# Kernel optimization log

Hardware: AMD Instinct MI355X
Metric: run time of the kernel (lower is better)

## Reference

```python
import jax, jax.numpy as jnp
import numpy as np

B = 4096          # batch
F = 1024          # feature_count * embedding_dim
E = 16            # embedding_dim (domain embedding)
D = 8             # num_domains
T = F + E         # cross-net total dim
L = 3             # cross layers
EPS = 1e-5


def setup_inputs() -> dict:
    key = jax.random.key(0)
    ks = jax.random.split(key, 32)
    s = 0.02
    inp = {}
    inp["x"] = jax.random.normal(ks[0], (B, F), dtype=jnp.float32)
    inp["domain_ids"] = jax.random.randint(ks[1], (B,), 0, D)
    # partitioned normalization params
    inp["pn_weight"] = jnp.ones((D, F), jnp.float32)
    inp["pn_bias"] = jnp.zeros((D, F), jnp.float32)
    # domain embedding table
    inp["dom_emb"] = jax.random.normal(ks[2], (D, E), jnp.float32) * 0.1
    # cross network: L layers, each Linear(T->1, no bias) + additive bias vector
    inp["cross_w"] = jax.random.normal(ks[3], (L, T), jnp.float32) * s
    inp["cross_b"] = jnp.zeros((L, T), jnp.float32)
    # center MLP: T->512->256->128 (ReLU, ReLU, none)
    inp["cW1"] = jax.random.normal(ks[4], (T, 512), jnp.float32) * s
    inp["cb1"] = jnp.zeros((512,), jnp.float32)
    inp["cW2"] = jax.random.normal(ks[5], (512, 256), jnp.float32) * s
    inp["cb2"] = jnp.zeros((256,), jnp.float32)
    inp["cW3"] = jax.random.normal(ks[6], (256, 128), jnp.float32) * s
    inp["cb3"] = jnp.zeros((128,), jnp.float32)
    # per-domain nets: T->512->256->128; last bias initialized to domain_net_init_bias=1.0
    inp["dW1"] = jax.random.normal(ks[7], (D, T, 512), jnp.float32) * s
    inp["db1"] = jnp.zeros((D, 512), jnp.float32)
    inp["dW2"] = jax.random.normal(ks[8], (D, 512, 256), jnp.float32) * s
    inp["db2"] = jnp.zeros((D, 256), jnp.float32)
    inp["dW3"] = jax.random.normal(ks[9], (D, 256, 128), jnp.float32) * s
    inp["db3"] = jnp.ones((D, 128), jnp.float32)
    # final MLP: 128->64->1
    inp["fW1"] = jax.random.normal(ks[10], (128, 64), jnp.float32) * s
    inp["fb1"] = jnp.zeros((64,), jnp.float32)
    inp["fW2"] = jax.random.normal(ks[11], (64, 1), jnp.float32) * s
    inp["fb2"] = jnp.zeros((1,), jnp.float32)
    # auxiliary net: E->32->1
    inp["aW1"] = jax.random.normal(ks[12], (E, 32), jnp.float32) * s
    inp["ab1"] = jnp.zeros((32,), jnp.float32)
    inp["aW2"] = jax.random.normal(ks[13], (32, 1), jnp.float32) * s
    inp["ab2"] = jnp.zeros((1,), jnp.float32)
    return inp


def _forward(x, domain_ids, pn_weight, pn_bias, dom_emb, cross_w, cross_b,
             cW1, cb1, cW2, cb2, cW3, cb3,
             dW1, db1, dW2, db2, dW3, db3,
             fW1, fb1, fW2, fb2, aW1, ab1, aW2, ab2):
    # --- PartitionedNormalization: per-sample LayerNorm stats + domain-indexed affine ---
    mean = jnp.mean(x, axis=1, keepdims=True)
    var = jnp.mean((x - mean) ** 2, axis=1, keepdims=True)  # unbiased=False
    normed = (x - mean) / jnp.sqrt(var + EPS)
    normed = normed * pn_weight[domain_ids] + pn_bias[domain_ids]

    xd = dom_emb[domain_ids]                    # (B, E)
    x0 = jnp.concatenate([normed, xd], axis=1)  # (B, T)

    # --- CrossNetworkWithDomain ---
    xc = x0
    for i in range(L):
        proj = xc @ cross_w[i]                  # (B,)
        xc = x0 * proj[:, None] + cross_b[i] + xc

    # --- center MLP ---
    h = jax.nn.relu(xc @ cW1 + cb1)
    h = jax.nn.relu(h @ cW2 + cb2)
    h_center = h @ cW3 + cb3                    # (B, 128)

    # --- domain-specific nets: run all D nets, select per-sample ---
    a = jax.nn.relu(jnp.einsum('bi,dio->bdo', xc, dW1) + db1[None])   # (B, D, 512)
    a = jax.nn.relu(jnp.einsum('bdi,dio->bdo', a, dW2) + db2[None])   # (B, D, 256)
    a = jnp.einsum('bdi,dio->bdo', a, dW3) + db3[None]                # (B, D, 128)
    h_domain = a[jnp.arange(a.shape[0]), domain_ids]                  # (B, 128)

    # --- STAR fusion (tanh) ---
    fused = h_center * jnp.tanh(h_domain)

    # --- final MLP + auxiliary net ---
    main_logits = jax.nn.relu(fused @ fW1 + fb1) @ fW2 + fb2          # (B, 1)
    aux_logits = jax.nn.relu(xd @ aW1 + ab1) @ aW2 + ab2              # (B, 1)
    return jax.nn.sigmoid(main_logits + aux_logits)


def reference(x, domain_ids, pn_weight, pn_bias, dom_emb, cross_w, cross_b,
              cW1, cb1, cW2, cb2, cW3, cb3,
              dW1, db1, dW2, db2, dW3, db3,
              fW1, fb1, fW2, fb2, aW1, ab1, aW2, ab2):
    return _forward(x, domain_ids, pn_weight, pn_bias, dom_emb, cross_w, cross_b,
                    cW1, cb1, cW2, cb2, cW3, cb3,
                    dW1, db1, dW2, db2, dW3, db3,
                    fW1, fb1, fW2, fb2, aW1, ab1, aW2, ab2)
```

## Files before the change

kernel.cpp:

```cpp
#include <hip/hip_runtime.h>
#include <math.h>
#include <stdint.h>

#define BATCH 4096
#define FEAT  1024
#define EDIM  16
#define NDOM  8
#define TDIM  1040
#define KP1   1088
#define NLAYER 3
#define EPSV  1e-5f

typedef __attribute__((ext_vector_type(8))) short bf16x8;
typedef __attribute__((ext_vector_type(4))) float f32x4;

__device__ __forceinline__ unsigned short f2bf(float f) {
    union { float f; unsigned int u; } v; v.f = f;
    unsigned int u = v.u;
    return (unsigned short)((u + 0x7fffu + ((u >> 16) & 1u)) >> 16);
}
__device__ __forceinline__ float bf2f(unsigned short u) {
    union { unsigned int u; float f; } v; v.u = ((unsigned int)u) << 16; return v.f;
}
__device__ __forceinline__ void gload_lds16(const void* g, void* l) {
    __builtin_amdgcn_global_load_lds(
        (const __attribute__((address_space(1))) void*)(g),
        (__attribute__((address_space(3))) void*)(l), 16, 0, 0);
}

#define T_W1 136
#define T_W2 32
#define T_W3 8
#define NCONV (T_W1*9 + T_W2*9 + T_W3*9)

__global__ __launch_bounds__(256) void front(
    const int* __restrict__ dom, int* __restrict__ perm, int* __restrict__ starts,
    const float* __restrict__ cW1, const float* __restrict__ dW1,
    const float* __restrict__ cW2, const float* __restrict__ dW2,
    const float* __restrict__ cW3, const float* __restrict__ dW3,
    unsigned short* __restrict__ Wc1b, unsigned short* __restrict__ Wd1b,
    unsigned short* __restrict__ Wc2b, unsigned short* __restrict__ Wd2b,
    unsigned short* __restrict__ Wc3b, unsigned short* __restrict__ Wd3b,
    const float* __restrict__ x,
    const float* __restrict__ pnw, const float* __restrict__ pnb,
    const float* __restrict__ demb,
    const float* __restrict__ crw, const float* __restrict__ crb,
    const float* __restrict__ aW1, const float* __restrict__ ab1,
    const float* __restrict__ aW2, const float* __restrict__ ab2,
    unsigned short* __restrict__ XCb, float* __restrict__ auxg) {
    int b = blockIdx.x;
    int t = threadIdx.x;

    if (b < NCONV) {
        __shared__ float tile[64][65];
        const float* src; unsigned short* dst; int K, N, Kp, rr;
        if (b < T_W1)            { src = cW1; dst = Wc1b; K = TDIM; N = 512; Kp = KP1; rr = b; }
        else if (b < T_W1*9)     { int r = b - T_W1; int z = r / T_W1; rr = r % T_W1;
                                   src = dW1 + (size_t)z * TDIM * 512; dst = Wd1b + (size_t)z * 512 * KP1;
                                   K = TDIM; N = 512; Kp = KP1; }
        else if (b < T_W1*9+T_W2)   { src = cW2; dst = Wc2b; K = 512; N = 256; Kp = 512; rr = b - T_W1*9; }
        else if (b < T_W1*9+T_W2*9) { int r = b - (T_W1*9+T_W2); int z = r / T_W2; rr = r % T_W2;
                                   src = dW2 + (size_t)z * 512 * 256; dst = Wd2b + (size_t)z * 256 * 512;
                                   K = 512; N = 256; Kp = 512; }
        else if (b < T_W1*9+T_W2*9+T_W3) { src = cW3; dst = Wc3b; K = 256; N = 128; Kp = 256; rr = b - (T_W1*9+T_W2*9); }
        else                     { int r = b - (T_W1*9+T_W2*9+T_W3); int z = r / T_W3; rr = r % T_W3;
                                   src = dW3 + (size_t)z * 256 * 128; dst = Wd3b + (size_t)z * 128 * 256;
                                   K = 256; N = 128; Kp = 256; }
        int kt = Kp >> 6;
        int kb = rr % kt, nb = rr / kt;
        int k0 = kb * 64, n0 = nb * 64;
        #pragma unroll
        for (int i = 0; i < 4; i++) {
            int flat = t + i * 256;
            int kr = flat >> 4, c4 = flat & 15;
            int k = k0 + kr;
            float4 v = make_float4(0.f, 0.f, 0.f, 0.f);
            if (k < K) v = *(const float4*)(src + (size_t)k * N + n0 + c4 * 4);
            tile[kr][c4 * 4 + 0] = v.x;
            tile[kr][c4 * 4 + 1] = v.y;
            tile[kr][c4 * 4 + 2] = v.z;
            tile[kr][c4 * 4 + 3] = v.w;
        }
        __syncthreads();
        #pragma unroll
        for (int i = 0; i < 4; i++) {
            int flat = t + i * 256;
            int n = flat >> 4, kg = flat & 15;
            ushort4 sv;
            sv.x = f2bf(tile[kg * 4 + 0][n]);
            sv.y = f2bf(tile[kg * 4 + 1][n]);
            sv.z = f2bf(tile[kg * 4 + 2][n]);
            sv.w = f2bf(tile[kg * 4 + 3][n]);
            *(ushort4*)(dst + (size_t)(n0 + n) * Kp + k0 + kg * 4) = sv;
        }
        return;
    }
    if (b == NCONV) {
        __shared__ int cnt[NDOM];
        __shared__ int off[NDOM];
        if (t < NDOM) cnt[t] = 0;
        __syncthreads();
        for (int i = t; i < BATCH; i += 256) atomicAdd(&cnt[dom[i]], 1);
        __syncthreads();
        if (t == 0) {
            int s = 0;
            for (int d = 0; d < NDOM; d++) { off[d] = s; starts[d] = s; s += cnt[d]; }
            starts[NDOM] = s;
        }
        __syncthreads();
        for (int i = t; i < BATCH; i += 256) {
            int p = atomicAdd(&off[dom[i]], 1);
            perm[p] = i;
        }
        return;
    }

    int w = t >> 6, lane = t & 63;
    int row = (b - NCONV - 1) * 4 + w;
    int d = dom[row];

    float4 X[4];
    #pragma unroll
    for (int j = 0; j < 4; j++)
        X[j] = *(const float4*)(x + (size_t)row * FEAT + 4 * lane + 256 * j);

    float s = 0.f, ss = 0.f;
    #pragma unroll
    for (int j = 0; j < 4; j++) {
        s  += X[j].x + X[j].y + X[j].z + X[j].w;
        ss += X[j].x*X[j].x + X[j].y*X[j].y + X[j].z*X[j].z + X[j].w*X[j].w;
    }
    #pragma unroll
    for (int m = 1; m < 64; m <<= 1) {
        s  += __shfl_xor(s,  m);
        ss += __shfl_xor(ss, m);
    }
    float mean = s / (float)FEAT;
    float var  = ss / (float)FEAT - mean * mean;
    float rstd = rsqrtf(var + EPSV);

    float4 x0[4], xc[4];
    #pragma unroll
    for (int j = 0; j < 4; j++) {
        float4 wv = *(const float4*)(pnw + (size_t)d * FEAT + 4 * lane + 256 * j);
        float4 bv = *(const float4*)(pnb + (size_t)d * FEAT + 4 * lane + 256 * j);
        x0[j].x = (X[j].x - mean) * rstd * wv.x + bv.x;
        x0[j].y = (X[j].y - mean) * rstd * wv.y + bv.y;
        x0[j].z = (X[j].z - mean) * rstd * wv.z + bv.z;
        x0[j].w = (X[j].w - mean) * rstd * wv.w + bv.w;
        xc[j] = x0[j];
    }
    float x0e = 0.f, xce = 0.f;
    if (lane < EDIM) { x0e = demb[d * EDIM + lane]; xce = x0e; }

    #pragma unroll
    for (int l = 0; l < NLAYER; l++) {
        const float* wl = crw + l * TDIM;
        const float* bl = crb + l * TDIM;
        float partial = 0.f;
        #pragma unroll
        for (int j = 0; j < 4; j++) {
            float4 wv = *(const float4*)(wl + 4 * lane + 256 * j);
            partial += xc[j].x*wv.x + xc[j].y*wv.y + xc[j].z*wv.z + xc[j].w*wv.w;
        }
        if (lane < EDIM) partial += xce * wl[FEAT + lane];
        #pragma unroll
        for (int m = 1; m < 64; m <<= 1) partial += __shfl_xor(partial, m);
        float proj = partial;
        #pragma unroll
        for (int j = 0; j < 4; j++) {
            float4 bv = *(const float4*)(bl + 4 * lane + 256 * j);
            xc[j].x = fmaf(x0[j].x, proj, bv.x + xc[j].x);
            xc[j].y = fmaf(x0[j].y, proj, bv.y + xc[j].y);
            xc[j].z = fmaf(x0[j].z, proj, bv.z + xc[j].z);
            xc[j].w = fmaf(x0[j].w, proj, bv.w + xc[j].w);
        }
        if (lane < EDIM) xce = fmaf(x0e, proj, bl[FEAT + lane] + xce);
    }

    #pragma unroll
    for (int j = 0; j < 4; j++) {
        ushort4 sv;
        sv.x = f2bf(xc[j].x); sv.y = f2bf(xc[j].y);
        sv.z = f2bf(xc[j].z); sv.w = f2bf(xc[j].w);
        *(ushort4*)(XCb + (size_t)row * KP1 + 4 * lane + 256 * j) = sv;
    }
    XCb[(size_t)row * KP1 + FEAT + lane] = (lane < EDIM) ? f2bf(xce) : 0;

    float h = (lane < 32) ? ab1[lane] : 0.f;
    #pragma unroll
    for (int e = 0; e < EDIM; e++) {
        float ev = __shfl(xce, e);
        if (lane < 32) h = fmaf(ev, aW1[e * 32 + lane], h);
    }
    float c = (lane < 32) ? fmaxf(h, 0.f) * aW2[lane] : 0.f;
    #pragma unroll
    for (int m = 1; m < 64; m <<= 1) c += __shfl_xor(c, m);
    if (lane == 0) auxg[row] = c + ab2[0];
}

__global__ __launch_bounds__(256) void gemm_mfma_v3(
    const unsigned short* __restrict__ Ac, const unsigned short* __restrict__ Ad, int lda,
    const unsigned short* __restrict__ Wc, const unsigned short* __restrict__ Wd,
    const float* __restrict__ bc, const float* __restrict__ bd,
    unsigned short* __restrict__ Cc, unsigned short* __restrict__ Cd,
    const int* __restrict__ starts, const int* __restrict__ perm, int usePerm,
    int Kp, int N, int relu) {
    __shared__ short As[128 * 64];
    __shared__ short Bs[64 * 64];

    const unsigned short* A; const unsigned short* W; const float* bias;
    unsigned short* C;
    int m0, mEnd;
    int y = blockIdx.y;
    if (y < 32) {
        A = Ac; W = Wc; bias = bc; C = Cc;
        m0 = y * 128; mEnd = BATCH;
    } else {
        int yy = y - 32;
        int d = yy >> 5, sl = yy & 31;
        int ds = starts[d], de = starts[d + 1];
        m0 = ds + sl * 128;
        if (m0 >= de) return;
        mEnd = de;
        A = Ad; W = Wd + (size_t)d * N * Kp; bias = bd + d * N; C = Cd;
    }
    int n0 = blockIdx.x * 64;
    int tid = threadIdx.x;
    int w = tid >> 6, lane = tid & 63;
    int wm = w >> 1, wn = w & 1;
    int lr = lane & 15, q = lane >> 4;

    const unsigned short* pA[4]; const unsigned short* pB[2];
    short* dA[4]; short* dB[2];
    #pragma unroll
    for (int i = 0; i < 4; i++) {
        int seg = i * 4 + w;
        int ch = seg * 64 + lane;
        int loc = ch >> 3, c = ch & 7;
        int mm = m0 + loc; if (mm > mEnd - 1) mm = mEnd - 1;
        int rowp = usePerm ? perm[mm] : mm;
        pA[i] = A + (size_t)rowp * lda + ((c ^ (loc & 7)) << 3);
        dA[i] = As + seg * 512;
    }
    #pragma unroll
    for (int i = 0; i < 2; i++) {
        int seg = i * 4 + w;
        int ch = seg * 64 + lane;
        int loc = ch >> 3, c = ch & 7;
        pB[i] = W + (size_t)(n0 + loc) * Kp + ((c ^ (loc & 7)) << 3);
        dB[i] = Bs + seg * 512;
    }

    f32x4 acc[4][2];
    #pragma unroll
    for (int i = 0; i < 4; i++)
        #pragma unroll
        for (int j = 0; j < 2; j++)
            acc[i][j] = (f32x4){0.f, 0.f, 0.f, 0.f};

    for (int k0 = 0; k0 < Kp; k0 += 64) {
        #pragma unroll
        for (int i = 0; i < 4; i++) gload_lds16(pA[i] + k0, dA[i]);
        #pragma unroll
        for (int i = 0; i < 2; i++) gload_lds16(pB[i] + k0, dB[i]);
        __syncthreads();

        #pragma unroll
        for (int half = 0; half < 2; half++) {
            int c = half * 4 + q;
            bf16x8 af[4], bf[2];
            #pragma unroll
            for (int i = 0; i < 4; i++) {
                int m = wm * 64 + i * 16 + lr;
                af[i] = *(const bf16x8*)(As + m * 64 + ((c ^ (m & 7)) << 3));
            }
            #pragma unroll
            for (int j = 0; j < 2; j++) {
                int n = wn * 32 + j * 16 + lr;
                bf[j] = *(const bf16x8*)(Bs + n * 64 + ((c ^ (n & 7)) << 3));
            }
            #pragma unroll
            for (int i = 0; i < 4; i++)
                #pragma unroll
                for (int j = 0; j < 2; j++)
                    acc[i][j] = __builtin_amdgcn_mfma_f32_16x16x32_bf16(
                        af[i], bf[j], acc[i][j], 0, 0, 0);
        }
        __syncthreads();
    }

    #pragma unroll
    for (int i = 0; i < 4; i++) {
        #pragma unroll
        for (int j = 0; j < 2; j++) {
            int col = n0 + wn * 32 + j * 16 + lr;
            float bvv = bias[col];
            int rowb = m0 + wm * 64 + i * 16 + q * 4;
            #pragma unroll
            for (int r = 0; r < 4; r++) {
                int row = rowb + r;
                if (row >= mEnd) continue;
                float val = acc[i][j][r] + bvv;
                if (relu) val = fmaxf(val, 0.f);
                C[(size_t)row * N + col] = f2bf(val);
            }
        }
    }
}

__global__ __launch_bounds__(256) void tail_fused(
    const unsigned short* __restrict__ H1c, const unsigned short* __restrict__ H1d,
    const unsigned short* __restrict__ Wc2, const unsigned short* __restrict__ Wd2,
    const float* __restrict__ cb2v, const float* __restrict__ db2v,
    const unsigned short* __restrict__ Wc3, const unsigned short* __restrict__ Wd3,
    const float* __restrict__ cb3v, const float* __restrict__ db3v,
    const float* __restrict__ fW1, const float* __restrict__ fb1,
    const float* __restrict__ fW2, const float* __restrict__ fb2,
    const float* __restrict__ auxg, const int* __restrict__ perm,
    const int* __restrict__ starts, float* __restrict__ out) {

    __shared__ __align__(16) char smem[98304];
    short* Bsb[2] = { (short*)smem, (short*)(smem + 32768) };
    short* Asb[2] = { (short*)(smem + 65536), (short*)(smem + 69632) };
    short* H2    = (short*)(smem + 73728);
    short* fused = (short*)(smem + 90112);

    int y = blockIdx.x;
    int d = y >> 7, sl = y & 127;
    int ds = starts[d], de = starts[d + 1];
    int m0 = ds + sl * 32;
    if (m0 >= de) return;
    int mEnd = de;

    int tid = threadIdx.x;
    int w = tid >> 6, lane = tid & 63;
    int lr = lane & 15, q = lane >> 4;

    int bn = w * 8 + (lane >> 3);
    int sw = ((lane & 7) ^ (bn & 7)) << 3;
    int rowA = m0 + bn; if (rowA > mEnd - 1) rowA = mEnd - 1;

    const unsigned short* pA0  = H1c + (size_t)rowA * 512 + sw;
    const unsigned short* pA1  = H1d + (size_t)rowA * 512 + sw;
    const unsigned short* pW20 = Wc2 + (size_t)bn * 512 + sw;
    const unsigned short* pW21 = Wd2 + (size_t)d * 256 * 512 + (size_t)bn * 512 + sw;
    const unsigned short* pW30 = Wc3 + (size_t)bn * 256 + sw;
    const unsigned short* pW31 = Wd3 + (size_t)d * 128 * 256 + (size_t)bn * 256 + sw;

    auto stage_l2 = [&](int c, int k0, int pb) {
        const unsigned short* pa = c ? pA1 : pA0;
        const unsigned short* pw = c ? pW21 : pW20;
        gload_lds16(pa + k0, Asb[pb] + w * 512);
        #pragma unroll
        for (int i = 0; i < 8; i++)
            gload_lds16(pw + (size_t)i * 32 * 512 + k0, Bsb[pb] + (i * 4 + w) * 512);
    };
    auto stage_l3 = [&](int c, int k0, int pb) {
        const unsigned short* pw = c ? pW31 : pW30;
        #pragma unroll
        for (int i = 0; i < 4; i++)
            gload_lds16(pw + (size_t)i * 32 * 256 + k0, Bsb[pb] + (i * 4 + w) * 512);
    };

    stage_l2(0, 0, 0);
    __syncthreads();

    #pragma unroll
    for (int c = 0; c < 2; c++) {
        f32x4 acc2[2][4];
        #pragma unroll
        for (int i = 0; i < 2; i++)
            #pragma unroll
            for (int j = 0; j < 4; j++) acc2[i][j] = (f32x4){0.f, 0.f, 0.f, 0.f};

        #pragma unroll
        for (int it = 0; it < 8; it++) {
            int t = c * 12 + it;
            int pb = t & 1, pn = pb ^ 1;
            if (it < 7) stage_l2(c, (it + 1) * 64, pn);
            else        stage_l3(c, 0, pn);

            #pragma unroll
            for (int half = 0; half < 2; half++) {
                int cc = half * 4 + q;
                bf16x8 af[2], bf[4];
                #pragma unroll
                for (int i = 0; i < 2; i++) {
                    int m = i * 16 + lr;
                    af[i] = *(const bf16x8*)(Asb[pb] + m * 64 + ((cc ^ (m & 7)) << 3));
                }
                #pragma unroll
                for (int j = 0; j < 4; j++) {
                    int n = w * 64 + j * 16 + lr;
                    bf[j] = *(const bf16x8*)(Bsb[pb] + n * 64 + ((cc ^ (n & 7)) << 3));
                }
                #pragma unroll
                for (int i = 0; i < 2; i++)
                    #pragma unroll
                    for (int j = 0; j < 4; j++)
                        acc2[i][j] = __builtin_amdgcn_mfma_f32_16x16x32_bf16(
                            af[i], bf[j], acc2[i][j], 0, 0, 0);
            }
            __syncthreads();
        }

        const float* b2 = c ? (db2v + d * 256) : cb2v;
        #pragma unroll
        for (int i = 0; i < 2; i++)
            #pragma unroll
            for (int j = 0; j < 4; j++) {
                int col = w * 64 + j * 16 + lr;
                float bv = b2[col];
                int cch = col >> 3;
                #pragma unroll
                for (int r = 0; r < 4; r++) {
                    int row = i * 16 + q * 4 + r;
                    int pc = (cch & 24) | ((cch ^ (row & 7)) & 7);
                    float v = fmaxf(acc2[i][j][r] + bv, 0.f);
                    H2[row * 256 + pc * 8 + (col & 7)] = (short)f2bf(v);
                }
            }
        __syncthreads();

        f32x4 acc3[2][2];
        #pragma unroll
        for (int i = 0; i < 2; i++)
            #pragma unroll
            for (int j = 0; j < 2; j++) acc3[i][j] = (f32x4){0.f, 0.f, 0.f, 0.f};

        #pragma unroll
        for (int it = 0; it < 4; it++) {
            int t = c * 12 + 8 + it;
            int pb = t & 1, pn = pb ^ 1;
            if (it < 3)      stage_l3(c, (it + 1) * 64, pn);
            else if (c == 0) stage_l2(1, 0, pn);

            #pragma unroll
            for (int half = 0; half < 2; half++) {
                int cc = half * 4 + q;
                int C = it * 8 + cc;
                bf16x8 af[2], bf[2];
                #pragma unroll
                for (int i = 0; i < 2; i++) {
                    int m = i * 16 + lr;
                    int pcm = (C & 24) | ((C ^ (m & 7)) & 7);
                    af[i] = *(const bf16x8*)(H2 + m * 256 + pcm * 8);
                }
                #pragma unroll
                for (int j = 0; j < 2; j++) {
                    int n = w * 32 + j * 16 + lr;
                    bf[j] = *(const bf16x8*)(Bsb[pb] + n * 64 + ((cc ^ (n & 7)) << 3));
                }
                #pragma unroll
                for (int i = 0; i < 2; i++)
                    #pragma unroll
                    for (int j = 0; j < 2; j++)
                        acc3[i][j] = __builtin_amdgcn_mfma_f32_16x16x32_bf16(
                            af[i], bf[j], acc3[i][j], 0, 0, 0);
            }
            __syncthreads();
        }

        const float* b3 = c ? (db3v + d * 128) : cb3v;
        #pragma unroll
        for (int i = 0; i < 2; i++)
            #pragma unroll
            for (int j = 0; j < 2; j++) {
                int col = w * 32 + j * 16 + lr;
                float bv = b3[col];
                int cch = col >> 3;
                #pragma unroll
                for (int r = 0; r < 4; r++) {
                    int row = i * 16 + q * 4 + r;
                    int pc = (cch & 8) | ((cch ^ (row & 7)) & 7);
                    int idx = row * 128 + pc * 8 + (col & 7);
                    if (c == 0) {
                        fused[idx] = (short)f2bf(acc3[i][j][r] + bv);
                    } else {
                        float cv = bf2f((unsigned short)fused[idx]);
                        fused[idx] = (short)f2bf(cv * tanhf(acc3[i][j][r] + bv));
                    }
                }
            }
        __syncthreads();
    }

    short* Bsf = Bsb[0];
    float* Ls  = (float*)Asb[0];
    for (int s2 = tid; s2 < 1024; s2 += 256) {
        int n = s2 >> 4, cch = s2 & 15;
        bf16x8 vv;
        #pragma unroll
        for (int kk = 0; kk < 8; kk++)
            vv[kk] = (short)f2bf(fW1[(cch * 8 + kk) * 64 + n]);
        int pc = (cch & 8) | ((cch ^ (n & 7)) & 7);
        *(bf16x8*)(Bsf + n * 128 + pc * 8) = vv;
    }
    __syncthreads();

    int wm = w >> 1, wn = w & 1;
    f32x4 acc2f[2];
    #pragma unroll
    for (int j = 0; j < 2; j++) acc2f[j] = (f32x4){0.f, 0.f, 0.f, 0.f};
    #pragma unroll
    for (int g = 0; g < 4; g++) {
        int cc = g * 4 + q;
        int m = wm * 16 + lr;
        int pcm = (cc & 8) | ((cc ^ (m & 7)) & 7);
        bf16x8 af = *(const bf16x8*)(fused + m * 128 + pcm * 8);
        #pragma unroll
        for (int j = 0; j < 2; j++) {
            int n = wn * 32 + j * 16 + lr;
            int pcn = (cc & 8) | ((cc ^ (n & 7)) & 7);
            bf16x8 bf = *(const bf16x8*)(Bsf + n * 128 + pcn * 8);
            acc2f[j] = __builtin_amdgcn_mfma_f32_16x16x32_bf16(af, bf, acc2f[j], 0, 0, 0);
        }
    }

    float w2v[2], b1v[2];
    #pragma unroll
    for (int j = 0; j < 2; j++) {
        int col = wn * 32 + j * 16 + lr;
        w2v[j] = fW2[col];
        b1v[j] = fb1[col];
    }
    float rowv[4];
    #pragma unroll
    for (int r = 0; r < 4; r++) {
        float v = 0.f;
        #pragma unroll
        for (int j = 0; j < 2; j++)
            v += fmaxf(acc2f[j][r] + b1v[j], 0.f) * w2v[j];
        v += __shfl_xor(v, 1);
        v += __shfl_xor(v, 2);
        v += __shfl_xor(v, 4);
        v += __shfl_xor(v, 8);
        rowv[r] = v;
    }
    if (wn == 0 && lr == 0) {
        #pragma unroll
        for (int r = 0; r < 4; r++)
            Ls[wm * 16 + q * 4 + r] = rowv[r];
    }
    __syncthreads();
    if (wn == 1 && lr == 0) {
        float b2 = fb2[0];
        #pragma unroll
        for (int r = 0; r < 4; r++) {
            int row = wm * 16 + q * 4 + r;
            int p = m0 + row;
            if (p < mEnd) {
                int orow = perm[p];
                float logit = Ls[row] + rowv[r] + b2 + auxg[orow];
                out[orow] = 1.f / (1.f + expf(-logit));
            }
        }
    }
}

extern "C" void kernel_launch(void* const* d_in, const int* in_sizes, int n_in,
                              void* d_out, int out_size, void* d_ws, size_t ws_size,
                              hipStream_t stream) {
    (void)in_sizes; (void)n_in; (void)out_size; (void)ws_size;

    const float* x    = (const float*)d_in[0];
    const int*   dom  = (const int*)  d_in[1];
    const float* pnw  = (const float*)d_in[2];
    const float* pnb  = (const float*)d_in[3];
    const float* demb = (const float*)d_in[4];
    const float* crw  = (const float*)d_in[5];
    const float* crb  = (const float*)d_in[6];
    const float* cW1  = (const float*)d_in[7];
    const float* cb1  = (const float*)d_in[8];
    const float* cW2  = (const float*)d_in[9];
    const float* cb2  = (const float*)d_in[10];
    const float* cW3  = (const float*)d_in[11];
    const float* cb3  = (const float*)d_in[12];
    const float* dW1  = (const float*)d_in[13];
    const float* db1  = (const float*)d_in[14];
    const float* dW2  = (const float*)d_in[15];
    const float* db2  = (const float*)d_in[16];
    const float* dW3  = (const float*)d_in[17];
    const float* db3  = (const float*)d_in[18];
    const float* fW1  = (const float*)d_in[19];
    const float* fb1  = (const float*)d_in[20];
    const float* fW2  = (const float*)d_in[21];
    const float* fb2  = (const float*)d_in[22];
    const float* aW1  = (const float*)d_in[23];
    const float* ab1  = (const float*)d_in[24];
    const float* aW2  = (const float*)d_in[25];
    const float* ab2  = (const float*)d_in[26];
    float* out = (float*)d_out;

    char* base = (char*)d_ws;
    size_t o = 0;
    auto alloc = [&](size_t bytes) { char* p = base + o; o += (bytes + 255) & ~size_t(255); return p; };

    int* perm   = (int*)alloc(BATCH * 4);
    int* starts = (int*)alloc((NDOM + 1) * 4);
    float* auxg = (float*)alloc(BATCH * 4);
    unsigned short* XCb  = (unsigned short*)alloc((size_t)BATCH * KP1 * 2);
    unsigned short* H1c  = (unsigned short*)alloc((size_t)BATCH * 512 * 2);
    unsigned short* H1d  = (unsigned short*)alloc((size_t)BATCH * 512 * 2);
    unsigned short* Wc1b = (unsigned short*)alloc((size_t)512 * KP1 * 2);
    unsigned short* Wd1b = (unsigned short*)alloc((size_t)NDOM * 512 * KP1 * 2);
    unsigned short* Wc2b = (unsigned short*)alloc((size_t)256 * 512 * 2);
    unsigned short* Wd2b = (unsigned short*)alloc((size_t)NDOM * 256 * 512 * 2);
    unsigned short* Wc3b = (unsigned short*)alloc((size_t)128 * 256 * 2);
    unsigned short* Wd3b = (unsigned short*)alloc((size_t)NDOM * 128 * 256 * 2);

    front<<<NCONV + 1 + BATCH / 4, 256, 0, stream>>>(
        dom, perm, starts, cW1, dW1, cW2, dW2, cW3, dW3,
        Wc1b, Wd1b, Wc2b, Wd2b, Wc3b, Wd3b,
        x, pnw, pnb, demb, crw, crb, aW1, ab1, aW2, ab2, XCb, auxg);

    gemm_mfma_v3<<<dim3(512 / 64, 32 + NDOM * 32), 256, 0, stream>>>(
        XCb, XCb, KP1, Wc1b, Wd1b, cb1, db1, H1c, H1d, starts, perm, 1, KP1, 512, 1);

    tail_fused<<<NDOM * 128, 256, 0, stream>>>(
        H1c, H1d, Wc2b, Wd2b, cb2, db2, Wc3b, Wd3b, cb3, db3,
        fW1, fb1, fW2, fb2, auxg, perm, starts, out);
}
```

Baseline: 197.0 us.

## Fuse center and domain layer-1 GEMMs so each A tile is loaded once

The layer-1 GEMM used to launch separate blocks for the center path and for each domain's rows, so every input row tile was fetched twice. Now each block loads one permuted A tile and a 128-wide B tile made of 64 center-weight columns and 64 domain-weight columns. It computes both outputs, with the wn wave half choosing center or domain for bias and output. This halves A traffic and removes the 32 extra center blocks, at the cost of twice the accumulators per wave (more register pressure) and a larger shared-memory tile.

```diff
diff --git a/kernel.cpp b/kernel.cpp
--- a/kernel.cpp
+++ b/kernel.cpp
@@ -199,111 +199,105 @@
     if (lane == 0) auxg[row] = c + ab2[0];
 }
 
-__global__ __launch_bounds__(256) void gemm_mfma_v3(
-    const unsigned short* __restrict__ Ac, const unsigned short* __restrict__ Ad, int lda,
-    const unsigned short* __restrict__ Wc, const unsigned short* __restrict__ Wd,
+__global__ __launch_bounds__(256) void gemm_l1_fused(
+    const unsigned short* __restrict__ A,
+    const unsigned short* __restrict__ Wc,
+    const unsigned short* __restrict__ Wd,
     const float* __restrict__ bc, const float* __restrict__ bd,
     unsigned short* __restrict__ Cc, unsigned short* __restrict__ Cd,
-    const int* __restrict__ starts, const int* __restrict__ perm, int usePerm,
-    int Kp, int N, int relu) {
+    const int* __restrict__ starts, const int* __restrict__ perm) {
     __shared__ short As[128 * 64];
-    __shared__ short Bs[64 * 64];
-
-    const unsigned short* A; const unsigned short* W; const float* bias;
-    unsigned short* C;
-    int m0, mEnd;
+    __shared__ short Bs[128 * 64];
+
     int y = blockIdx.y;
-    if (y < 32) {
-        A = Ac; W = Wc; bias = bc; C = Cc;
-        m0 = y * 128; mEnd = BATCH;
-    } else {
-        int yy = y - 32;
-        int d = yy >> 5, sl = yy & 31;
-        int ds = starts[d], de = starts[d + 1];
-        m0 = ds + sl * 128;
-        if (m0 >= de) return;
-        mEnd = de;
-        A = Ad; W = Wd + (size_t)d * N * Kp; bias = bd + d * N; C = Cd;
-    }
+    int d = y >> 5, sl = y & 31;
+    int ds = starts[d], de = starts[d + 1];
+    int m0 = ds + sl * 128;
+    if (m0 >= de) return;
+    int mEnd = de;
     int n0 = blockIdx.x * 64;
+
     int tid = threadIdx.x;
     int w = tid >> 6, lane = tid & 63;
     int wm = w >> 1, wn = w & 1;
     int lr = lane & 15, q = lane >> 4;
 
-    const unsigned short* pA[4]; const unsigned short* pB[2];
-    short* dA[4]; short* dB[2];
+    const unsigned short* pA[4]; short* dA[4];
+    const unsigned short* pB[4]; short* dB[4];
     #pragma unroll
     for (int i = 0; i < 4; i++) {
         int seg = i * 4 + w;
         int ch = seg * 64 + lane;
         int loc = ch >> 3, c = ch & 7;
         int mm = m0 + loc; if (mm > mEnd - 1) mm = mEnd - 1;
-        int rowp = usePerm ? perm[mm] : mm;
-        pA[i] = A + (size_t)rowp * lda + ((c ^ (loc & 7)) << 3);
+        int rowp = perm[mm];
+        pA[i] = A + (size_t)rowp * KP1 + ((c ^ (loc & 7)) << 3);
         dA[i] = As + seg * 512;
     }
     #pragma unroll
-    for (int i = 0; i < 2; i++) {
+    for (int i = 0; i < 4; i++) {
         int seg = i * 4 + w;
         int ch = seg * 64 + lane;
         int loc = ch >> 3, c = ch & 7;
-        pB[i] = W + (size_t)(n0 + loc) * Kp + ((c ^ (loc & 7)) << 3);
+        const unsigned short* base = (loc < 64)
+            ? (Wc + (size_t)(n0 + loc) * KP1)
+            : (Wd + ((size_t)d * 512 + n0 + (loc - 64)) * KP1);
+        pB[i] = base + ((c ^ (loc & 7)) << 3);
         dB[i] = Bs + seg * 512;
     }
 
-    f32x4 acc[4][2];
+    f32x4 acc[4][4];
     #pragma unroll
     for (int i = 0; i < 4; i++)
         #pragma unroll
-        for (int j = 0; j < 2; j++)
+        for (int j = 0; j < 4; j++)
             acc[i][j] = (f32x4){0.f, 0.f, 0.f, 0.f};
 
-    for (int k0 = 0; k0 < Kp; k0 += 64) {
+    for (int k0 = 0; k0 < KP1; k0 += 64) {
         #pragma unroll
         for (int i = 0; i < 4; i++) gload_lds16(pA[i] + k0, dA[i]);
         #pragma unroll
-        for (int i = 0; i < 2; i++) gload_lds16(pB[i] + k0, dB[i]);
+        for (int i = 0; i < 4; i++) gload_lds16(pB[i] + k0, dB[i]);
         __syncthreads();
 
         #pragma unroll
         for (int half = 0; half < 2; half++) {
-            int c = half * 4 + q;
-            bf16x8 af[4], bf[2];
+            int cc = half * 4 + q;
+            bf16x8 af[4], bf[4];
             #pragma unroll
             for (int i = 0; i < 4; i++) {
                 int m = wm * 64 + i * 16 + lr;
-                af[i] = *(const bf16x8*)(As + m * 64 + ((c ^ (m & 7)) << 3));
-            }
-            #pragma unroll
-            for (int j = 0; j < 2; j++) {
-                int n = wn * 32 + j * 16 + lr;
-                bf[j] = *(const bf16x8*)(Bs + n * 64 + ((c ^ (n & 7)) << 3));
+                af[i] = *(const bf16x8*)(As + m * 64 + ((cc ^ (m & 7)) << 3));
+            }
+            #pragma unroll
+            for (int j = 0; j < 4; j++) {
+                int n = wn * 64 + j * 16 + lr;
+                bf[j] = *(const bf16x8*)(Bs + n * 64 + ((cc ^ (n & 7)) << 3));
             }
             #pragma unroll
             for (int i = 0; i < 4; i++)
                 #pragma unroll
-                for (int j = 0; j < 2; j++)
+                for (int j = 0; j < 4; j++)
                     acc[i][j] = __builtin_amdgcn_mfma_f32_16x16x32_bf16(
                         af[i], bf[j], acc[i][j], 0, 0, 0);
         }
         __syncthreads();
     }
 
+    const float* bias = wn ? (bd + d * 512) : bc;
+    unsigned short* C = wn ? Cd : Cc;
     #pragma unroll
     for (int i = 0; i < 4; i++) {
         #pragma unroll
-        for (int j = 0; j < 2; j++) {
-            int col = n0 + wn * 32 + j * 16 + lr;
+        for (int j = 0; j < 4; j++) {
+            int col = n0 + j * 16 + lr;
             float bvv = bias[col];
             int rowb = m0 + wm * 64 + i * 16 + q * 4;
             #pragma unroll
             for (int r = 0; r < 4; r++) {
                 int row = rowb + r;
                 if (row >= mEnd) continue;
-                float val = acc[i][j][r] + bvv;
-                if (relu) val = fmaxf(val, 0.f);
-                C[(size_t)row * N + col] = f2bf(val);
+                C[(size_t)row * 512 + col] = f2bf(fmaxf(acc[i][j][r] + bvv, 0.f));
             }
         }
     }
@@ -615,8 +609,8 @@
         Wc1b, Wd1b, Wc2b, Wd2b, Wc3b, Wd3b,
         x, pnw, pnb, demb, crw, crb, aW1, ab1, aW2, ab2, XCb, auxg);
 
-    gemm_mfma_v3<<<dim3(512 / 64, 32 + NDOM * 32), 256, 0, stream>>>(
-        XCb, XCb, KP1, Wc1b, Wd1b, cb1, db1, H1c, H1d, starts, perm, 1, KP1, 512, 1);
+    gemm_l1_fused<<<dim3(512 / 64, NDOM * 32), 256, 0, stream>>>(
+        XCb, Wc1b, Wd1b, cb1, db1, H1c, H1d, starts, perm);
 
     tail_fused<<<NDOM * 128, 256, 0, stream>>>(
         H1c, H1d, Wc2b, Wd2b, cb2, db2, Wc3b, Wd3b, cb3, db3,
```

After: 191.8 us. 2.7% less time.
